# Performance work log

Measured on AMD Instinct MI355X. Metric: run time of the kernel, lower is better.

## Reference

```python
import jax, jax.numpy as jnp
import numpy as np

EPS = 1e-6  # RMSNorm eps (torch nn.RMSNorm with fp32 default eps ~ machine eps; 1e-6 used here)


def _rmsnorm(x, w):
    return x * jax.lax.rsqrt(jnp.mean(x * x, axis=-1, keepdims=True) + EPS) * w


def _mamba_block(x, norm_w, in_proj_w, conv_w, conv_b, x_proj_w, dt_proj_w,
                 dt_proj_b, A_log, D_param, out_proj_w):
    # x: (B, L, D). NanoSSSM: MambaBlock(RMSNorm(x)), NO residual.
    B, L, D = x.shape
    K = conv_w.shape[1]            # d_conv
    N = A_log.shape[1]             # d_state
    dt_rank = dt_proj_w.shape[0]
    h = _rmsnorm(x, norm_w)
    xz = h @ in_proj_w             # (B, L, 2*ED)
    xi, z = jnp.split(xz, 2, axis=-1)
    # depthwise causal conv1d over L (kernel K, left pad K-1, truncate to L)
    xp = jnp.pad(xi, ((0, 0), (K - 1, 0), (0, 0)))
    xc = sum(xp[:, k:k + L, :] * conv_w[:, k] for k in range(K)) + conv_b
    xi = jax.nn.silu(xc)
    dbc = xi @ x_proj_w            # (B, L, dt_rank + 2N)
    delta = jax.nn.softplus(dbc[..., :dt_rank] @ dt_proj_w + dt_proj_b)  # (B,L,ED)
    Bm = dbc[..., dt_rank:dt_rank + N]   # (B, L, N)
    Cm = dbc[..., dt_rank + N:]          # (B, L, N)
    A = -jnp.exp(A_log)                  # (ED, N)
    deltaA = jnp.exp(delta[..., None] * A)                   # (B, L, ED, N)
    BX = (delta * xi)[..., None] * Bm[:, :, None, :]         # (B, L, ED, N)

    def _comb(c1, c2):
        a1, b1 = c1
        a2, b2 = c2
        return a1 * a2, a2 * b1 + b2

    # parallel selective scan: h_t = deltaA_t * h_{t-1} + BX_t
    _, hs = jax.lax.associative_scan(_comb, (deltaA, BX), axis=1)
    y = jnp.einsum('blen,bln->ble', hs, Cm) + D_param * xi
    y = y * jax.nn.silu(z)
    return y @ out_proj_w


def setup_inputs() -> dict:
    key = jax.random.key(0)
    ks = jax.random.split(key, 12)
    B, L = 4, 2048
    VOCAB, EMB, D = 6400, 512, 768
    ED, N, dt_rank, K = 768, 1, 48, 1
    s = 0.02
    return {
        "tokens": jax.random.randint(ks[0], (B, L), 0, VOCAB),
        "n_layers": 8,
        "emb_table": jax.random.normal(ks[1], (VOCAB, EMB)) * s,
        "emb_proj_w": jax.random.normal(ks[2], (EMB, D)) * s,
        "norm_w": jnp.ones((D,)),
        "in_proj_w": jax.random.normal(ks[3], (D, 2 * ED)) * s,
        "conv_w": jax.random.normal(ks[4], (ED, K)) * s,
        "conv_b": jnp.zeros((ED,)),
        "x_proj_w": jax.random.normal(ks[5], (ED, dt_rank + 2 * N)) * s,
        "dt_proj_w": jax.random.normal(ks[6], (dt_rank, ED)) * s,
        "dt_proj_b": jnp.zeros((ED,)),
        "A_log": jnp.log(jnp.tile(jnp.arange(1, N + 1, dtype=jnp.float32), (ED, 1))),
        "D_param": jnp.ones((ED,)),
        "out_proj_w": jax.random.normal(ks[7], (ED, D)) * s,
        "out_norm_w": jnp.ones((D,)),
        "head_w": jax.random.normal(ks[8], (D, VOCAB)) * s,
        "head_b": jnp.zeros((VOCAB,)),
    }


def reference(tokens, n_layers, emb_table, emb_proj_w, norm_w, in_proj_w,
              conv_w, conv_b, x_proj_w, dt_proj_w, dt_proj_b, A_log, D_param,
              out_proj_w, out_norm_w, head_w, head_b):
    x = emb_table[tokens] @ emb_proj_w  # NanoEmbedding
    # NanoLLM reuses the SAME block instance n_layers times (weight tying)
    for _ in range(n_layers):
        x = _mamba_block(x, norm_w, in_proj_w, conv_w, conv_b, x_proj_w,
                         dt_proj_w, dt_proj_b, A_log, D_param, out_proj_w)
    return _rmsnorm(x, out_norm_w) @ head_w + head_b  # NanoOutput
```

## Files before the change

kernel.cpp:

```cpp
#include <hip/hip_runtime.h>
#include <math.h>

#define TQ    8192
#define DM    768
#define EMBD  512
#define NVOC  6400
#define LSEQ  2048
#define NBAT  4
#define NLAYER 8
#define DTR   48
#define CHUNK 32
#define NCH   (LSEQ/CHUNK)

typedef float f32x16  __attribute__((ext_vector_type(16)));
typedef short bf16x8  __attribute__((ext_vector_type(8)));
typedef short short4v __attribute__((ext_vector_type(4)));

static __device__ __forceinline__ short f2bf(float x) {
    unsigned u = __float_as_uint(x);
    unsigned r = (u + 0x7fffu + ((u >> 16) & 1u)) >> 16;
    return (short)r;
}
static __device__ __forceinline__ float bf2f(short h) {
    return __uint_as_float(((unsigned)(unsigned short)h) << 16);
}
static __device__ __forceinline__ void split4(float4 v, short4v& h4, short4v& m4, short4v& l4)
{
    float x0 = v.x, x1 = v.y, x2 = v.z, x3 = v.w;
#define SPL(i, xx) { short h = f2bf(xx); float r = (xx) - bf2f(h);              \
                     short m = f2bf(r);  float r2 = r - bf2f(m);                \
                     short l = f2bf(r2); h4[i] = h; m4[i] = m; l4[i] = l; }
    SPL(0, x0) SPL(1, x1) SPL(2, x2) SPL(3, x3)
#undef SPL
}
static __device__ __forceinline__ void split1(float x, short& h, short& m, short& l)
{
    h = f2bf(x); float r = x - bf2f(h);
    m = f2bf(r); float r2 = r - bf2f(m);
    l = f2bf(r2);
}

#define BM 128
#define KS 32
#define ASTR 40

template<int NMF, int BNT, bool BIAS, bool CONVSILU>
__global__ __launch_bounds__(256)
void gemmp_k(const short* __restrict__ Ap, int lda, size_t strideA,
             const short* __restrict__ Bp, int ldb, size_t strideB,
             float* __restrict__ C, int ldc,
             int M, int N, int kslice,
             const float* __restrict__ bias,
             const float* __restrict__ cw, const float* __restrict__ cb,
             short* __restrict__ xip, size_t strideXip,
             size_t slab)
{
    constexpr int NPLA = (NMF >= 6) ? 3 : (NMF == 2 ? 1 : 2);
    constexpr int NPLB = (NMF >= 6) ? 3 : 2;
    constexpr int NCT = BNT / 64;
    __shared__ __align__(16) short Asl[NPLA][BM * ASTR];
    __shared__ __align__(16) short Bsl[NPLB][BNT * ASTR];

    const int tid = threadIdx.x;
    const int ln  = tid & 63;
    const int wid = tid >> 6;
    const int wr  = wid >> 1;
    const int wc  = wid & 1;
    const int m0  = blockIdx.x * BM;
    const int n0  = blockIdx.y * BNT;
    const int kbeg = blockIdx.z * kslice;
    float* Cz = C + (size_t)blockIdx.z * slab;

    const int frow = ln & 31;
    const int h8   = (ln >> 5) * 8;

    f32x16 acc[2][NCT];
#pragma unroll
    for (int i = 0; i < 2; ++i)
#pragma unroll
        for (int j = 0; j < NCT; ++j) acc[i][j] = (f32x16)0.f;

    for (int k0 = kbeg; k0 < kbeg + kslice; k0 += KS) {
        __syncthreads();
        bf16x8 av[2][NPLA], bv[NCT][NPLB];
#pragma unroll
        for (int i = 0; i < 2; ++i) {
            int u = tid + i * 256;
            int r = u >> 2, k8 = (u & 3) * 8;
            const short* ap = Ap + (size_t)(m0 + r) * lda + k0 + k8;
#pragma unroll
            for (int pl = 0; pl < NPLA; ++pl)
                av[i][pl] = *(const bf16x8*)(ap + pl * strideA);
        }
#pragma unroll
        for (int i = 0; i < NCT; ++i) {
            int u = tid + i * 256;
            int r = u >> 2, k8 = (u & 3) * 8;
            int nn = n0 + r;
            if (nn < N) {
                const short* bp = Bp + (size_t)nn * ldb + k0 + k8;
#pragma unroll
                for (int pl = 0; pl < NPLB; ++pl)
                    bv[i][pl] = *(const bf16x8*)(bp + pl * strideB);
            } else {
#pragma unroll
                for (int pl = 0; pl < NPLB; ++pl)
                    bv[i][pl] = (bf16x8)(short)0;
            }
        }
#pragma unroll
        for (int i = 0; i < 2; ++i) {
            int u = tid + i * 256;
            int r = u >> 2, k8 = (u & 3) * 8;
            int base = r * ASTR + k8;
#pragma unroll
            for (int pl = 0; pl < NPLA; ++pl)
                *(bf16x8*)&Asl[pl][base] = av[i][pl];
        }
#pragma unroll
        for (int i = 0; i < NCT; ++i) {
            int u = tid + i * 256;
            int r = u >> 2, k8 = (u & 3) * 8;
            int base = r * ASTR + k8;
#pragma unroll
            for (int pl = 0; pl < NPLB; ++pl)
                *(bf16x8*)&Bsl[pl][base] = bv[i][pl];
        }
        __syncthreads();
#pragma unroll
        for (int kg = 0; kg < 2; ++kg) {
            bf16x8 af[2][NPLA], bf[NCT][NPLB];
#pragma unroll
            for (int mt = 0; mt < 2; ++mt) {
                int off = (wr * 64 + mt * 32 + frow) * ASTR + kg * 16 + h8;
#pragma unroll
                for (int pl = 0; pl < NPLA; ++pl)
                    af[mt][pl] = *(const bf16x8*)&Asl[pl][off];
            }
#pragma unroll
            for (int ct = 0; ct < NCT; ++ct) {
                int off = (wc * (BNT / 2) + ct * 32 + frow) * ASTR + kg * 16 + h8;
#pragma unroll
                for (int pl = 0; pl < NPLB; ++pl)
                    bf[ct][pl] = *(const bf16x8*)&Bsl[pl][off];
            }
#pragma unroll
            for (int mt = 0; mt < 2; ++mt)
#pragma unroll
                for (int ct = 0; ct < NCT; ++ct) {
                    if (NMF == 6) {
                        acc[mt][ct] = __builtin_amdgcn_mfma_f32_32x32x16_bf16(af[mt][0], bf[ct][2], acc[mt][ct], 0, 0, 0);
                        acc[mt][ct] = __builtin_amdgcn_mfma_f32_32x32x16_bf16(af[mt][2], bf[ct][0], acc[mt][ct], 0, 0, 0);
                        acc[mt][ct] = __builtin_amdgcn_mfma_f32_32x32x16_bf16(af[mt][1], bf[ct][1], acc[mt][ct], 0, 0, 0);
                        acc[mt][ct] = __builtin_amdgcn_mfma_f32_32x32x16_bf16(af[mt][0], bf[ct][1], acc[mt][ct], 0, 0, 0);
                        acc[mt][ct] = __builtin_amdgcn_mfma_f32_32x32x16_bf16(af[mt][1], bf[ct][0], acc[mt][ct], 0, 0, 0);
                        acc[mt][ct] = __builtin_amdgcn_mfma_f32_32x32x16_bf16(af[mt][0], bf[ct][0], acc[mt][ct], 0, 0, 0);
                    } else if (NMF == 4) {
                        acc[mt][ct] = __builtin_amdgcn_mfma_f32_32x32x16_bf16(af[mt][1], bf[ct][1], acc[mt][ct], 0, 0, 0);
                        acc[mt][ct] = __builtin_amdgcn_mfma_f32_32x32x16_bf16(af[mt][0], bf[ct][1], acc[mt][ct], 0, 0, 0);
                        acc[mt][ct] = __builtin_amdgcn_mfma_f32_32x32x16_bf16(af[mt][1], bf[ct][0], acc[mt][ct], 0, 0, 0);
                        acc[mt][ct] = __builtin_amdgcn_mfma_f32_32x32x16_bf16(af[mt][0], bf[ct][0], acc[mt][ct], 0, 0, 0);
                    } else if (NMF == 3) {
                        acc[mt][ct] = __builtin_amdgcn_mfma_f32_32x32x16_bf16(af[mt][0], bf[ct][1], acc[mt][ct], 0, 0, 0);
                        acc[mt][ct] = __builtin_amdgcn_mfma_f32_32x32x16_bf16(af[mt][1], bf[ct][0], acc[mt][ct], 0, 0, 0);
                        acc[mt][ct] = __builtin_amdgcn_mfma_f32_32x32x16_bf16(af[mt][0], bf[ct][0], acc[mt][ct], 0, 0, 0);
                    } else {
                        acc[mt][ct] = __builtin_amdgcn_mfma_f32_32x32x16_bf16(af[mt][0], bf[ct][1], acc[mt][ct], 0, 0, 0);
                        acc[mt][ct] = __builtin_amdgcn_mfma_f32_32x32x16_bf16(af[mt][0], bf[ct][0], acc[mt][ct], 0, 0, 0);
                    }
                }
        }
    }

#pragma unroll
    for (int mt = 0; mt < 2; ++mt)
#pragma unroll
        for (int ct = 0; ct < NCT; ++ct) {
            int col = n0 + wc * (BNT / 2) + ct * 32 + (ln & 31);
            if (col < N) {
                int rbase = m0 + wr * 64 + mt * 32 + (ln >> 5) * 4;
                float cwv = 0.f, cbv = 0.f, bvs = 0.f;
                if (BIAS) bvs = bias[col];
                bool doconv = CONVSILU && (col < DM);
                if (doconv) { cwv = cw[col]; cbv = cb[col]; }
#pragma unroll
                for (int r = 0; r < 16; ++r) {
                    int row = rbase + (r & 3) + (r >> 2) * 8;
                    float v = acc[mt][ct][r];
                    if (BIAS) v += bvs;
                    if (doconv) {
                        float xc = fmaf(v, cwv, cbv);
                        v = xc / (1.f + expf(-xc));
                        short hh, mm, ll;
                        split1(v, hh, mm, ll);
                        size_t o = (size_t)row * DM + col;
                        xip[o] = hh;
                        xip[o + strideXip] = mm;
                        if (NPLB == 3) xip[o + 2 * strideXip] = ll;
                    } else {
                        Cz[(long)row * ldc + col] = v;
                    }
                }
            }
        }
}

#define OBM 128
#define OBN 128
#define OKS 32
#define OASTR 40

template<bool GATHER, bool ASCALE, bool BIAS>
__global__ __launch_bounds__(256)
void gemm_k(const float* __restrict__ A, int lda,
            const float* __restrict__ Bw,
            float* __restrict__ C, int ldc,
            int M, int N, int K,
            const int* __restrict__ rowidx,
            const float* __restrict__ rscale,
            const float* __restrict__ cscale,
            const float* __restrict__ bias)
{
    __shared__ __align__(16) short Ap[3][OBM * OASTR];
    __shared__ __align__(16) short Bp[3][OBN * OASTR];

    const int tid = threadIdx.x;
    const int ln  = tid & 63;
    const int wid = tid >> 6;
    const int wr  = wid >> 1;
    const int wc  = wid & 1;
    const int m0  = blockIdx.x * OBM;
    const int n0  = blockIdx.y * OBN;
    const bool fullN = (n0 + OBN <= N);

    const int frow = ln & 31;
    const int h8   = (ln >> 5) * 8;

    f32x16 acc[2][2];
#pragma unroll
    for (int i = 0; i < 2; ++i)
#pragma unroll
        for (int j = 0; j < 2; ++j) acc[i][j] = (f32x16)0.f;

    const int am  = tid >> 3;
    const int ak4 = (tid & 7) * 4;
    const int bkb = (tid >> 6) * 4;
    const int bn2 = (tid & 63) * 2;

    for (int k0 = 0; k0 < K; k0 += OKS) {
        __syncthreads();
#pragma unroll
        for (int p = 0; p < 4; ++p) {
            int m = am + p * 32;
            long grow = GATHER ? (long)rowidx[m0 + m] : (long)(m0 + m);
            float4 v = *(const float4*)&A[grow * lda + k0 + ak4];
            if (ASCALE) {
                float rsv = rscale[m0 + m];
                v.x *= rsv * cscale[k0 + ak4 + 0];
                v.y *= rsv * cscale[k0 + ak4 + 1];
                v.z *= rsv * cscale[k0 + ak4 + 2];
                v.w *= rsv * cscale[k0 + ak4 + 3];
            }
            short4v h4, m4, l4;
            split4(v, h4, m4, l4);
            int base = m * OASTR + ak4;
            *(short4v*)&Ap[0][base] = h4;
            *(short4v*)&Ap[1][base] = m4;
            *(short4v*)&Ap[2][base] = l4;
        }
#pragma unroll
        for (int p = 0; p < 2; ++p) {
            int kb = bkb + p * 16;
            float vv[4][2];
            if (fullN) {
#pragma unroll
                for (int i = 0; i < 4; ++i) {
                    float2 w = *(const float2*)&Bw[(long)(k0 + kb + i) * N + n0 + bn2];
                    vv[i][0] = w.x; vv[i][1] = w.y;
                }
            } else {
#pragma unroll
                for (int i = 0; i < 4; ++i)
#pragma unroll
                    for (int c = 0; c < 2; ++c) {
                        int ng = n0 + bn2 + c;
                        vv[i][c] = (ng < N) ? Bw[(long)(k0 + kb + i) * N + ng] : 0.f;
                    }
            }
#pragma unroll
            for (int c = 0; c < 2; ++c) {
                float4 t; t.x = vv[0][c]; t.y = vv[1][c]; t.z = vv[2][c]; t.w = vv[3][c];
                short4v h4, m4, l4;
                split4(t, h4, m4, l4);
                int base = (bn2 + c) * OASTR + kb;
                *(short4v*)&Bp[0][base] = h4;
                *(short4v*)&Bp[1][base] = m4;
                *(short4v*)&Bp[2][base] = l4;
            }
        }
        __syncthreads();
#pragma unroll
        for (int kg = 0; kg < 2; ++kg) {
            bf16x8 af[2][3], bf[2][3];
#pragma unroll
            for (int mt = 0; mt < 2; ++mt) {
                int off = (wr * 64 + mt * 32 + frow) * OASTR + kg * 16 + h8;
#pragma unroll
                for (int pl = 0; pl < 3; ++pl)
                    af[mt][pl] = *(const bf16x8*)&Ap[pl][off];
            }
#pragma unroll
            for (int nt = 0; nt < 2; ++nt) {
                int off = (wc * 64 + nt * 32 + frow) * OASTR + kg * 16 + h8;
#pragma unroll
                for (int pl = 0; pl < 3; ++pl)
                    bf[nt][pl] = *(const bf16x8*)&Bp[pl][off];
            }
#pragma unroll
            for (int mt = 0; mt < 2; ++mt)
#pragma unroll
                for (int nt = 0; nt < 2; ++nt) {
                    acc[mt][nt] = __builtin_amdgcn_mfma_f32_32x32x16_bf16(af[mt][0], bf[nt][2], acc[mt][nt], 0, 0, 0);
                    acc[mt][nt] = __builtin_amdgcn_mfma_f32_32x32x16_bf16(af[mt][2], bf[nt][0], acc[mt][nt], 0, 0, 0);
                    acc[mt][nt] = __builtin_amdgcn_mfma_f32_32x32x16_bf16(af[mt][1], bf[nt][1], acc[mt][nt], 0, 0, 0);
                    acc[mt][nt] = __builtin_amdgcn_mfma_f32_32x32x16_bf16(af[mt][0], bf[nt][1], acc[mt][nt], 0, 0, 0);
                    acc[mt][nt] = __builtin_amdgcn_mfma_f32_32x32x16_bf16(af[mt][1], bf[nt][0], acc[mt][nt], 0, 0, 0);
                    acc[mt][nt] = __builtin_amdgcn_mfma_f32_32x32x16_bf16(af[mt][0], bf[nt][0], acc[mt][nt], 0, 0, 0);
                }
        }
    }
#pragma unroll
    for (int mt = 0; mt < 2; ++mt)
#pragma unroll
        for (int nt = 0; nt < 2; ++nt) {
            int col = n0 + wc * 64 + nt * 32 + (ln & 31);
            if (col < N) {
                int rbase = m0 + wr * 64 + mt * 32 + (ln >> 5) * 4;
                float bvs = BIAS ? bias[col] : 0.f;
#pragma unroll
                for (int r = 0; r < 16; ++r) {
                    int row = rbase + (r & 3) + (r >> 2) * 8;
                    float v = acc[mt][nt][r];
                    if (BIAS) v += bvs;
                    C[(long)row * ldc + col] = v;
                }
            }
        }
}

__global__ __launch_bounds__(256)
void wsplit_k(const float* __restrict__ W, int K, int N,
              short* __restrict__ P, size_t pstride)
{
    __shared__ float Ws[64][65];
    int nt = blockIdx.x * 64, kt = blockIdx.y * 64;
    for (int u = threadIdx.x; u < 4096; u += 256) {
        int kk = u >> 6, nn = u & 63;
        Ws[kk][nn] = (nt + nn < N) ? W[(size_t)(kt + kk) * N + nt + nn] : 0.f;
    }
    __syncthreads();
    int nl = threadIdx.x >> 2, k16 = (threadIdx.x & 3) * 16;
    int n = nt + nl;
    if (n < N) {
        bf16x8 h[2], m[2], l[2];
#pragma unroll
        for (int j = 0; j < 16; ++j) {
            short hh, mm, ll;
            split1(Ws[k16 + j][nl], hh, mm, ll);
            h[j >> 3][j & 7] = hh; m[j >> 3][j & 7] = mm; l[j >> 3][j & 7] = ll;
        }
        size_t base = (size_t)n * K + kt + k16;
        *(bf16x8*)&P[base]              = h[0];
        *(bf16x8*)&P[base + 8]          = h[1];
        *(bf16x8*)&P[base + pstride]     = m[0];
        *(bf16x8*)&P[base + pstride + 8] = m[1];
        *(bf16x8*)&P[base + 2*pstride]     = l[0];
        *(bf16x8*)&P[base + 2*pstride + 8] = l[1];
    }
}

template<int NPW>
__global__ __launch_bounds__(256)
void rowsplit_k(const float* __restrict__ X, const float* __restrict__ cscale,
                float* __restrict__ rs, short* __restrict__ P, size_t pstride)
{
    int row  = blockIdx.x * 4 + (threadIdx.x >> 6);
    int lane = threadIdx.x & 63;
    const float4* xr = (const float4*)(X + (size_t)row * DM);
    float4 v[3];
    float s = 0.f;
#pragma unroll
    for (int e = 0; e < 3; ++e) {
        v[e] = xr[lane + e * 64];
        s = fmaf(v[e].x, v[e].x, s); s = fmaf(v[e].y, v[e].y, s);
        s = fmaf(v[e].z, v[e].z, s); s = fmaf(v[e].w, v[e].w, s);
    }
#pragma unroll
    for (int off = 1; off < 64; off <<= 1) s += __shfl_xor(s, off);
    float rsv = rsqrtf(s * (1.0f / DM) + 1e-6f);
    if (lane == 0) rs[row] = rsv;
#pragma unroll
    for (int e = 0; e < 3; ++e) {
        int k = (lane + e * 64) * 4;
        float4 w = v[e];
        w.x *= rsv * cscale[k + 0]; w.y *= rsv * cscale[k + 1];
        w.z *= rsv * cscale[k + 2]; w.w *= rsv * cscale[k + 3];
        short4v h4, m4, l4;
        split4(w, h4, m4, l4);
        size_t o = (size_t)row * DM + k;
        *(short4v*)&P[o] = h4;
        if (NPW >= 2) *(short4v*)&P[o + pstride]     = m4;
        if (NPW == 3) *(short4v*)&P[o + 2 * pstride] = l4;
    }
}

template<int NPX>
__global__ __launch_bounds__(256)
void dtscan_k(const float* __restrict__ part,
              const float* __restrict__ Wdt, const float* __restrict__ bdt,
              const short* __restrict__ XIp, size_t strideX,
              const float* __restrict__ Alog,
              float* __restrict__ a_out, float* __restrict__ bx_out,
              float* __restrict__ Ac, float* __restrict__ Sc,
              float* __restrict__ Cvb)
{
    __shared__ float ds[CHUNK][52];
    const int chg = blockIdx.x;
    const int t0  = chg * CHUNK;
    const int e   = blockIdx.y * 256 + threadIdx.x;

    for (int idx = threadIdx.x; idx < CHUNK * 50; idx += 256) {
        int tt = idx / 50, c = idx - tt * 50;
        size_t o = (size_t)(t0 + tt) * 50 + c;
        ds[tt][c] = part[o] + part[o + (size_t)TQ * 50]
                  + part[o + 2 * (size_t)TQ * 50] + part[o + 3 * (size_t)TQ * 50];
    }
    __syncthreads();
    if (blockIdx.y == 0 && threadIdx.x < CHUNK)
        Cvb[t0 + threadIdx.x] = ds[threadIdx.x][49];

    const float bias = bdt[e];
    const float An = -expf(Alog[e]);
    float Achunk = 1.f, Schunk = 0.f;

    for (int tb = 0; tb < CHUNK; tb += 16) {
        float acc[16];
#pragma unroll
        for (int tt = 0; tt < 16; ++tt) acc[tt] = bias;
        for (int k = 0; k < DTR; ++k) {
            float w = Wdt[(size_t)k * DM + e];
#pragma unroll
            for (int tt = 0; tt < 16; ++tt) acc[tt] = fmaf(ds[tb + tt][k], w, acc[tt]);
        }
#pragma unroll
        for (int tt = 0; tt < 16; ++tt) {
            int t = t0 + tb + tt;
            float delta = log1pf(expf(acc[tt]));
            float a  = expf(delta * An);
            size_t xidx = (size_t)t * DM + e;
            float xi = bf2f(XIp[xidx]) + bf2f(XIp[xidx + strideX]);
            if (NPX == 3) xi += bf2f(XIp[xidx + 2 * strideX]);
            float Bv = ds[tb + tt][48];
            float bxv = delta * xi * Bv;
            a_out [xidx] = a;
            bx_out[xidx] = bxv;
            Schunk = fmaf(a, Schunk, bxv);
            Achunk *= a;
        }
    }
    Ac[(size_t)chg * DM + e] = Achunk;
    Sc[(size_t)chg * DM + e] = Schunk;
}

template<int NPX, int NPW>
__global__ __launch_bounds__(256)
void scany_k(const float* __restrict__ a, const float* __restrict__ bx,
             const float* __restrict__ Ac, const float* __restrict__ Sc,
             const short* __restrict__ XIp, size_t strideX,
             const float* __restrict__ XZ, const float* __restrict__ Cvb,
             const float* __restrict__ Dp,
             short* __restrict__ Yp, size_t pstride)
{
    int gid = blockIdx.x * 256 + threadIdx.x;
    int e  = gid % DM;
    int bc = gid / DM;
    int ch = bc % NCH, b = bc / NCH;
    float h = 0.f;
    for (int c2 = 0; c2 < ch; ++c2) {
        size_t i = ((size_t)(b * NCH + c2)) * DM + e;
        h = fmaf(Ac[i], h, Sc[i]);
    }
    float Dv = Dp[e];
    int tbase = b * LSEQ + ch * CHUNK;
    for (int i = 0; i < CHUNK; ++i) {
        int t = tbase + i;
        size_t idx = (size_t)t * DM + e;
        h = fmaf(a[idx], h, bx[idx]);
        float Cv = Cvb[t];
        float xi = bf2f(XIp[idx]) + bf2f(XIp[idx + strideX]);
        if (NPX == 3) xi += bf2f(XIp[idx + 2 * strideX]);
        float z  = XZ[(size_t)t * 1536 + DM + e];
        float y  = fmaf(h, Cv, Dv * xi);
        float sz = z / (1.f + expf(-z));
        float yo = y * sz;
        short hh, mm, ll;
        split1(yo, hh, mm, ll);
        Yp[idx] = hh;
        Yp[idx + pstride] = mm;
        if (NPW == 3) Yp[idx + 2 * pstride] = ll;
    }
}

extern "C" void kernel_launch(void* const* d_in, const int* in_sizes, int n_in,
                              void* d_out, int out_size, void* d_ws, size_t ws_size,
                              hipStream_t stream)
{
    const int*   tokens   = (const int*)  d_in[0];
    const float* emb_tab  = (const float*)d_in[2];
    const float* emb_proj = (const float*)d_in[3];
    const float* norm_w   = (const float*)d_in[4];
    const float* in_proj  = (const float*)d_in[5];
    const float* conv_w   = (const float*)d_in[6];
    const float* conv_b   = (const float*)d_in[7];
    const float* x_proj   = (const float*)d_in[8];
    const float* dt_proj  = (const float*)d_in[9];
    const float* dt_b     = (const float*)d_in[10];
    const float* A_log    = (const float*)d_in[11];
    const float* D_param  = (const float*)d_in[12];
    const float* out_proj = (const float*)d_in[13];
    const float* out_norm = (const float*)d_in[14];
    const float* head_w   = (const float*)d_in[15];
    const float* head_b   = (const float*)d_in[16];

    float* Xbuf = (float*)d_ws;
    float* rs   = Xbuf + (size_t)TQ * DM;
    float* Ac   = rs + TQ;
    float* Sc   = Ac + (size_t)NBAT * NCH * DM;
    float* Cvb  = Sc + (size_t)NBAT * NCH * DM;
    short* wsEnd = (short*)(Cvb + TQ);

    float* XZ   = (float*)d_out;
    float* Abuf = XZ + (size_t)TQ * 1536;
    float* BX   = Abuf + (size_t)TQ * DM;
    float* PART = BX + (size_t)TQ * DM;
    short* SP   = (short*)(PART + (size_t)4 * TQ * 50);
    const size_t sWEP = (size_t)768 * EMBD;
    const size_t sWIP = (size_t)1536 * DM;
    const size_t sWXP = (size_t)50 * DM;
    const size_t sWOP = (size_t)DM * DM;
    const size_t sACT = (size_t)TQ * DM;
    short* WEPp = SP;
    short* WIPp = WEPp + 3 * sWEP;
    short* WXPp = WIPp + 3 * sWIP;
    short* WOPp = WXPp + 3 * sWXP;
    short* XIp  = WOPp + 3 * sWOP;
    short* XNp  = XIp + 3 * sACT;

    const size_t sWHD = (size_t)NVOC * DM;
    const size_t WS_BASE = (size_t)TQ * DM * 4 + TQ * 4 + 2 * (size_t)NBAT * NCH * DM * 4
                         + (size_t)TQ * 4;
    const size_t WS_NEED = WS_BASE + 3 * sACT * 2 + 3 * sWHD * 2;
    const bool wsok = (ws_size >= WS_NEED);
    short* XNhp = wsok ? wsEnd : XNp;
    short* WHDp = wsok ? (wsEnd + 3 * sACT) : (short*)nullptr;

    dim3 blk(256);

    wsplit_k<<<dim3(12, 8),  blk, 0, stream>>>(emb_proj, EMBD, DM,   WEPp, sWEP);
    wsplit_k<<<dim3(24, 12), blk, 0, stream>>>(in_proj,  DM, 1536,   WIPp, sWIP);
    wsplit_k<<<dim3(1, 12),  blk, 0, stream>>>(x_proj,   DM, 50,     WXPp, sWXP);
    wsplit_k<<<dim3(12, 12), blk, 0, stream>>>(out_proj, DM, DM,     WOPp, sWOP);
    if (wsok)
        wsplit_k<<<dim3(100, 12), blk, 0, stream>>>(head_w, DM, NVOC, WHDp, sWHD);

    gemm_k<true, false, false><<<dim3(TQ / OBM, DM / OBN), blk, 0, stream>>>(
        emb_tab, EMBD, emb_proj, Xbuf, DM, TQ, DM, EMBD,
        tokens, nullptr, nullptr, nullptr);

    for (int l = 0; l < NLAYER; ++l) {
        if (l < 3) {
            rowsplit_k<3><<<TQ / 4, blk, 0, stream>>>(Xbuf, norm_w, rs, XNp, sACT);
            gemmp_k<6, 128, false, true><<<dim3(TQ / BM, 1536 / 128), blk, 0, stream>>>(
                XNp, DM, sACT, WIPp, DM, sWIP, XZ, 1536, TQ, 1536, DM,
                nullptr, conv_w, conv_b, XIp, sACT, 0);
            gemmp_k<6, 64, false, false><<<dim3(TQ / BM, 1, 4), blk, 0, stream>>>(
                XIp, DM, sACT, WXPp, DM, sWXP, PART, 50, TQ, 50, DM / 4,
                nullptr, nullptr, nullptr, nullptr, 0, (size_t)TQ * 50);
            dtscan_k<3><<<dim3(TQ / CHUNK, DM / 256), blk, 0, stream>>>(
                PART, dt_proj, dt_b, XIp, sACT, A_log, Abuf, BX, Ac, Sc, Cvb);
            scany_k<3, 3><<<(NBAT * NCH * DM) / 256, blk, 0, stream>>>(
                Abuf, BX, Ac, Sc, XIp, sACT, XZ, Cvb, D_param, XNp, sACT);
            gemmp_k<6, 128, false, false><<<dim3(TQ / BM, DM / 128), blk, 0, stream>>>(
                XNp, DM, sACT, WOPp, DM, sWOP, Xbuf, DM, TQ, DM, DM,
                nullptr, nullptr, nullptr, nullptr, 0, 0);
        } else if (l == 3) {
            rowsplit_k<2><<<TQ / 4, blk, 0, stream>>>(Xbuf, norm_w, rs, XNp, sACT);
            gemmp_k<4, 128, false, true><<<dim3(TQ / BM, 1536 / 128), blk, 0, stream>>>(
                XNp, DM, sACT, WIPp, DM, sWIP, XZ, 1536, TQ, 1536, DM,
                nullptr, conv_w, conv_b, XIp, sACT, 0);
            gemmp_k<4, 64, false, false><<<dim3(TQ / BM, 1, 4), blk, 0, stream>>>(
                XIp, DM, sACT, WXPp, DM, sWXP, PART, 50, TQ, 50, DM / 4,
                nullptr, nullptr, nullptr, nullptr, 0, (size_t)TQ * 50);
            dtscan_k<2><<<dim3(TQ / CHUNK, DM / 256), blk, 0, stream>>>(
                PART, dt_proj, dt_b, XIp, sACT, A_log, Abuf, BX, Ac, Sc, Cvb);
            scany_k<2, 2><<<(NBAT * NCH * DM) / 256, blk, 0, stream>>>(
                Abuf, BX, Ac, Sc, XIp, sACT, XZ, Cvb, D_param, XNp, sACT);
            gemmp_k<4, 128, false, false><<<dim3(TQ / BM, DM / 128), blk, 0, stream>>>(
                XNp, DM, sACT, WOPp, DM, sWOP, Xbuf, DM, TQ, DM, DM,
                nullptr, nullptr, nullptr, nullptr, 0, 0);
        } else {
            rowsplit_k<2><<<TQ / 4, blk, 0, stream>>>(Xbuf, norm_w, rs, XNp, sACT);
            gemmp_k<3, 128, false, true><<<dim3(TQ / BM, 1536 / 128), blk, 0, stream>>>(
                XNp, DM, sACT, WIPp, DM, sWIP, XZ, 1536, TQ, 1536, DM,
                nullptr, conv_w, conv_b, XIp, sACT, 0);
            gemmp_k<3, 64, false, false><<<dim3(TQ / BM, 1, 4), blk, 0, stream>>>(
                XIp, DM, sACT, WXPp, DM, sWXP, PART, 50, TQ, 50, DM / 4,
                nullptr, nullptr, nullptr, nullptr, 0, (size_t)TQ * 50);
            dtscan_k<2><<<dim3(TQ / CHUNK, DM / 256), blk, 0, stream>>>(
                PART, dt_proj, dt_b, XIp, sACT, A_log, Abuf, BX, Ac, Sc, Cvb);
            scany_k<2, 2><<<(NBAT * NCH * DM) / 256, blk, 0, stream>>>(
                Abuf, BX, Ac, Sc, XIp, sACT, XZ, Cvb, D_param, XNp, sACT);
            gemmp_k<3, 128, false, false><<<dim3(TQ / BM, DM / 128), blk, 0, stream>>>(
                XNp, DM, sACT, WOPp, DM, sWOP, Xbuf, DM, TQ, DM, DM,
                nullptr, nullptr, nullptr, nullptr, 0, 0);
        }
    }

    if (wsok) {
        rowsplit_k<1><<<TQ / 4, blk, 0, stream>>>(Xbuf, out_norm, rs, XNhp, sACT);
        gemmp_k<2, 128, true, false><<<dim3(TQ / BM, NVOC / 128), blk, 0, stream>>>(
            XNhp, DM, sACT, WHDp, DM, sWHD, (float*)d_out, NVOC, TQ, NVOC, DM,
            head_b, nullptr, nullptr, nullptr, 0, 0);
    } else {
        rowsplit_k<1><<<TQ / 4, blk, 0, stream>>>(Xbuf, out_norm, rs, XNhp, sACT);
        gemm_k<false, true, true><<<dim3(TQ / OBM, NVOC / OBN), blk, 0, stream>>>(
            Xbuf, DM, head_w, (float*)d_out, NVOC, TQ, NVOC, DM,
            nullptr, rs, out_norm, head_b);
    }

    (void)in_sizes; (void)n_in; (void)out_size;
}
```

Baseline: 2.317 ms.

## Prefetch next K tile into registers during MFMA and swizzle block rows

The GEMM main loop now issues the global loads for the next K tile into registers right after the shared-memory store barrier, so they overlap with the MFMA work on the current tile. This replaces the earlier pattern of loading and then immediately storing within each iteration. Block row indices are also remapped in groups of 8 to change which tiles run concurrently, aiming for better cache locality. The prefetch raises register pressure, which may reduce occupancy, and the remap assumes gridDim.x is divisible by 8.

```diff
diff --git a/kernel.cpp b/kernel.cpp
--- a/kernel.cpp
+++ b/kernel.cpp
@@ -66,7 +66,9 @@
     const int wid = tid >> 6;
     const int wr  = wid >> 1;
     const int wc  = wid & 1;
-    const int m0  = blockIdx.x * BM;
+    const int gx  = gridDim.x >> 3;
+    const int bx  = blockIdx.x;
+    const int m0  = ((bx & 7) * gx + (bx >> 3)) * BM;
     const int n0  = blockIdx.y * BNT;
     const int kbeg = blockIdx.z * kslice;
     float* Cz = C + (size_t)blockIdx.z * slab;
@@ -80,34 +82,40 @@
 #pragma unroll
         for (int j = 0; j < NCT; ++j) acc[i][j] = (f32x16)0.f;
 
-    for (int k0 = kbeg; k0 < kbeg + kslice; k0 += KS) {
+    bf16x8 av[2][NPLA], bv[NCT][NPLB];
+
+#define LOADT(K0) do {                                                          \
+    _Pragma("unroll")                                                           \
+    for (int i_ = 0; i_ < 2; ++i_) {                                            \
+        int u_ = tid + i_ * 256;                                                \
+        int r_ = u_ >> 2, k8_ = (u_ & 3) * 8;                                   \
+        const short* ap_ = Ap + (size_t)(m0 + r_) * lda + (K0) + k8_;           \
+        _Pragma("unroll")                                                       \
+        for (int pl_ = 0; pl_ < NPLA; ++pl_)                                    \
+            av[i_][pl_] = *(const bf16x8*)(ap_ + pl_ * strideA);                \
+    }                                                                           \
+    _Pragma("unroll")                                                           \
+    for (int i_ = 0; i_ < NCT; ++i_) {                                          \
+        int u_ = tid + i_ * 256;                                                \
+        int r_ = u_ >> 2, k8_ = (u_ & 3) * 8;                                   \
+        int nn_ = n0 + r_;                                                      \
+        if (nn_ < N) {                                                          \
+            const short* bp_ = Bp + (size_t)nn_ * ldb + (K0) + k8_;             \
+            _Pragma("unroll")                                                   \
+            for (int pl_ = 0; pl_ < NPLB; ++pl_)                                \
+                bv[i_][pl_] = *(const bf16x8*)(bp_ + pl_ * strideB);            \
+        } else {                                                                \
+            _Pragma("unroll")                                                   \
+            for (int pl_ = 0; pl_ < NPLB; ++pl_)                                \
+                bv[i_][pl_] = (bf16x8)(short)0;                                 \
+        }                                                                       \
+    }                                                                           \
+} while (0)
+
+    LOADT(kbeg);
+    const int nk = kslice / KS;
+    for (int it = 0; it < nk; ++it) {
         __syncthreads();
-        bf16x8 av[2][NPLA], bv[NCT][NPLB];
-#pragma unroll
-        for (int i = 0; i < 2; ++i) {
-            int u = tid + i * 256;
-            int r = u >> 2, k8 = (u & 3) * 8;
-            const short* ap = Ap + (size_t)(m0 + r) * lda + k0 + k8;
-#pragma unroll
-            for (int pl = 0; pl < NPLA; ++pl)
-                av[i][pl] = *(const bf16x8*)(ap + pl * strideA);
-        }
-#pragma unroll
-        for (int i = 0; i < NCT; ++i) {
-            int u = tid + i * 256;
-            int r = u >> 2, k8 = (u & 3) * 8;
-            int nn = n0 + r;
-            if (nn < N) {
-                const short* bp = Bp + (size_t)nn * ldb + k0 + k8;
-#pragma unroll
-                for (int pl = 0; pl < NPLB; ++pl)
-                    bv[i][pl] = *(const bf16x8*)(bp + pl * strideB);
-            } else {
-#pragma unroll
-                for (int pl = 0; pl < NPLB; ++pl)
-                    bv[i][pl] = (bf16x8)(short)0;
-            }
-        }
 #pragma unroll
         for (int i = 0; i < 2; ++i) {
             int u = tid + i * 256;
@@ -127,6 +135,7 @@
                 *(bf16x8*)&Bsl[pl][base] = bv[i][pl];
         }
         __syncthreads();
+        if (it + 1 < nk) LOADT(kbeg + (it + 1) * KS);
 #pragma unroll
         for (int kg = 0; kg < 2; ++kg) {
             bf16x8 af[2][NPLA], bf[NCT][NPLB];
@@ -171,6 +180,7 @@
                 }
         }
     }
+#undef LOADT
 
 #pragma unroll
     for (int mt = 0; mt < 2; ++mt)
```

New measurement: 2.294 ms. Within noise of the previous version (-1.0%).
